# Performance work log

Measured on AMD Instinct MI355X. Metric: run time of the kernel, lower is better.

The kernel has to match this reference:

```python
import math
import jax, jax.numpy as jnp
import numpy as np

B = 32
L_ENC = 1024
LABEL = 512
PRED = 512
L_DEC = LABEL + PRED
ENC_IN = 7
C_OUT = 7
MARK = 4
D_MODEL = 512
N_HEADS = 8
D_FF = 2048
N_ENC = 2
N_DEC = 1
FACTOR = 1
MA = 25


def setup_inputs() -> dict:
    key = jax.random.key(0)
    ks = iter(jax.random.split(key, 40))
    def g(shape, scale=0.02):
        return jax.random.normal(next(ks), shape, dtype=jnp.float32) * scale
    inp = {}
    inp["x_enc"] = jax.random.normal(next(ks), (B, L_ENC, ENC_IN), dtype=jnp.float32)
    inp["x_mark_enc"] = jax.random.normal(next(ks), (B, L_ENC, MARK), dtype=jnp.float32)
    inp["x_dec"] = jax.random.normal(next(ks), (B, L_DEC, ENC_IN), dtype=jnp.float32)
    inp["x_mark_dec"] = jax.random.normal(next(ks), (B, L_DEC, MARK), dtype=jnp.float32)
    inp["W_enc_tok"] = g((3, ENC_IN, D_MODEL))
    inp["W_enc_tem"] = g((MARK, D_MODEL))
    inp["W_dec_tok"] = g((3, ENC_IN, D_MODEL))
    inp["W_dec_tem"] = g((MARK, D_MODEL))
    inp["enc_attn_W"] = g((N_ENC, 4, D_MODEL, D_MODEL))
    inp["enc_attn_b"] = jnp.zeros((N_ENC, 4, D_MODEL), jnp.float32)
    inp["enc_ff1"] = g((N_ENC, D_MODEL, D_FF))
    inp["enc_ff2"] = g((N_ENC, D_FF, D_MODEL))
    inp["enc_ln_w"] = jnp.ones((D_MODEL,), jnp.float32)
    inp["enc_ln_b"] = jnp.zeros((D_MODEL,), jnp.float32)
    inp["dec_self_W"] = g((N_DEC, 4, D_MODEL, D_MODEL))
    inp["dec_self_b"] = jnp.zeros((N_DEC, 4, D_MODEL), jnp.float32)
    inp["dec_cross_W"] = g((N_DEC, 4, D_MODEL, D_MODEL))
    inp["dec_cross_b"] = jnp.zeros((N_DEC, 4, D_MODEL), jnp.float32)
    inp["dec_ff1"] = g((N_DEC, D_MODEL, D_FF))
    inp["dec_ff2"] = g((N_DEC, D_FF, D_MODEL))
    inp["dec_trend_W"] = g((N_DEC, 3, D_MODEL, C_OUT))
    inp["dec_ln_w"] = jnp.ones((D_MODEL,), jnp.float32)
    inp["dec_ln_b"] = jnp.zeros((D_MODEL,), jnp.float32)
    inp["proj_W"] = g((D_MODEL, C_OUT))
    inp["proj_b"] = jnp.zeros((C_OUT,), jnp.float32)
    return inp


def moving_mean(x, k):
    # AvgPool1d(kernel=k, stride=1) over time with edge-replication padding (k odd)
    pad = (k - 1) // 2
    xp = jnp.concatenate([jnp.repeat(x[:, :1], pad, axis=1), x, jnp.repeat(x[:, -1:], pad, axis=1)], axis=1)
    cs = jnp.concatenate([jnp.zeros_like(xp[:, :1]), jnp.cumsum(xp, axis=1)], axis=1)
    return (cs[:, k:] - cs[:, :-k]) / k


def series_decomp(x, k=MA):
    m = moving_mean(x, k)
    return x - m, m


def my_layernorm(x, w, b):
    # LayerNorm over features, then subtract per-series seasonal bias (mean over time)
    mu = jnp.mean(x, axis=-1, keepdims=True)
    var = jnp.var(x, axis=-1, keepdims=True)
    xh = (x - mu) / jnp.sqrt(var + 1e-5) * w + b
    return xh - jnp.mean(xh, axis=1, keepdims=True)


def circ_conv3(x, W):
    # Conv1d kernel=3, circular padding, no bias; W: (3, c_in, c_out)
    xp = jnp.concatenate([x[:, -1:], x, x[:, :1]], axis=1)
    return xp[:, :-2] @ W[0] + xp[:, 1:-1] @ W[1] + xp[:, 2:] @ W[2]


def autocorrelation(q, k, v):
    # q: (B,L,H,E); k,v: (B,S,H,E)
    B_, L, H, E = q.shape
    S = v.shape[1]
    if L > S:
        pad = jnp.zeros((B_, L - S, H, E), q.dtype)
        k = jnp.concatenate([k, pad], axis=1)
        v = jnp.concatenate([v, pad], axis=1)
    else:
        k = k[:, :L]
        v = v[:, :L]
    qf = jnp.fft.rfft(jnp.transpose(q, (0, 2, 3, 1)), axis=-1)
    kf = jnp.fft.rfft(jnp.transpose(k, (0, 2, 3, 1)), axis=-1)
    corr = jnp.fft.irfft(qf * jnp.conj(kf), n=L, axis=-1)  # (B,H,E,L)
    vals = jnp.transpose(v, (0, 2, 3, 1))  # (B,H,E,L)
    top_k = int(FACTOR * math.log(L))
    mean_value = jnp.mean(corr, axis=(1, 2))  # (B,L)
    weights, delay = jax.lax.top_k(mean_value, top_k)
    tmp_corr = jax.nn.softmax(weights, axis=-1)  # (B,top_k)
    t_idx = jnp.arange(L)
    out = jnp.zeros_like(vals)
    for i in range(top_k):  # small fixed loop (top_k ~ log L)
        idx = (t_idx[None, :] + delay[:, i:i + 1]) % L  # (B,L) circular roll indices
        pat = jnp.take_along_axis(vals, idx[:, None, None, :], axis=-1)
        out = out + pat * tmp_corr[:, i][:, None, None, None]
    return jnp.transpose(out, (0, 3, 1, 2))  # (B,L,H,E)


def attn_layer(xq, xk, xv, W, b):
    Bq, L, _ = xq.shape
    S = xk.shape[1]
    q = (xq @ W[0] + b[0]).reshape(Bq, L, N_HEADS, -1)
    k = (xk @ W[1] + b[1]).reshape(Bq, S, N_HEADS, -1)
    v = (xv @ W[2] + b[2]).reshape(Bq, S, N_HEADS, -1)
    o = autocorrelation(q, k, v).reshape(Bq, L, -1)
    return o @ W[3] + b[3]


def reference(x_enc, x_mark_enc, x_dec, x_mark_dec, W_enc_tok, W_enc_tem, W_dec_tok, W_dec_tem, enc_attn_W, enc_attn_b, enc_ff1, enc_ff2, enc_ln_w, enc_ln_b, dec_self_W, dec_self_b, dec_cross_W, dec_cross_b, dec_ff1, dec_ff2, dec_trend_W, dec_ln_w, dec_ln_b, proj_W, proj_b):
    mean = jnp.broadcast_to(jnp.mean(x_enc, axis=1, keepdims=True), (x_enc.shape[0], PRED, x_enc.shape[2]))
    zeros = jnp.zeros((x_dec.shape[0], PRED, x_dec.shape[2]), x_enc.dtype)
    seasonal_init, trend_init = series_decomp(x_enc)
    trend_init = jnp.concatenate([trend_init[:, -LABEL:], mean], axis=1)
    seasonal_init = jnp.concatenate([seasonal_init[:, -LABEL:], zeros], axis=1)
    # embeddings (token conv + timeF linear; dropout=0 -> identity)
    enc = circ_conv3(x_enc, W_enc_tok) + x_mark_enc @ W_enc_tem
    for l in range(N_ENC):
        enc = enc + attn_layer(enc, enc, enc, enc_attn_W[l], enc_attn_b[l])
        enc, _ = series_decomp(enc)
        y = jax.nn.gelu(enc @ enc_ff1[l], approximate=False) @ enc_ff2[l]
        enc, _ = series_decomp(enc + y)
    enc = my_layernorm(enc, enc_ln_w, enc_ln_b)
    dec = circ_conv3(seasonal_init, W_dec_tok) + x_mark_dec @ W_dec_tem
    trend = trend_init
    for l in range(N_DEC):
        dec = dec + attn_layer(dec, dec, dec, dec_self_W[l], dec_self_b[l])
        dec, t1 = series_decomp(dec)
        dec = dec + attn_layer(dec, enc, enc, dec_cross_W[l], dec_cross_b[l])
        dec, t2 = series_decomp(dec)
        y = jax.nn.gelu(dec @ dec_ff1[l], approximate=False) @ dec_ff2[l]
        dec, t3 = series_decomp(dec + y)
        trend = trend + circ_conv3(t1 + t2 + t3, dec_trend_W[l])
    dec = my_layernorm(dec, dec_ln_w, dec_ln_b)
    seasonal = dec @ proj_W + proj_b
    return (trend + seasonal)[:, -PRED:]
```

## Files before the change

kernel.cpp:

```cpp
#include <hip/hip_runtime.h>

typedef unsigned short ushortb;
typedef __attribute__((ext_vector_type(8))) _Float16 f16x8;
typedef __attribute__((ext_vector_type(4))) float f32x4;

__device__ __forceinline__ float h2f(ushortb u) {
    _Float16 h; __builtin_memcpy(&h, &u, 2); return (float)h;
}
__device__ __forceinline__ ushortb f2h(float f) {
    _Float16 h = (_Float16)f; ushortb u; __builtin_memcpy(&u, &h, 2); return u;
}
__device__ __forceinline__ float gelu_f(float x) {
    float z = x * (1.59576912f + 0.0713548128f * x * x);
    return x / (1.f + __expf(-z));
}

__device__ __forceinline__ void ld16(const void* g, void* l) {
    __builtin_amdgcn_global_load_lds(
        (const __attribute__((address_space(1))) unsigned int*)g,
        (__attribute__((address_space(3))) unsigned int*)l, 16, 0, 0);
}

__device__ __forceinline__ void xcd_remap(int& bx, int& by) {
    int nx = gridDim.x;
    int total = nx * gridDim.y;
    bx = blockIdx.x; by = blockIdx.y;
    if ((total & 7) == 0) {
        int lin = by * nx + bx;
        int lin2 = (lin & 7) * (total >> 3) + (lin >> 3);
        by = lin2 / nx; bx = lin2 % nx;
    }
}

__launch_bounds__(256)
__global__ void gemm_h3(const ushortb* __restrict__ Ah, const ushortb* __restrict__ Al,
                        int lda,
                        const ushortb* __restrict__ Bh, const ushortb* __restrict__ Bl,
                        int ldb,
                        const float* __restrict__ bias,
                        ushortb* __restrict__ Ch, ushortb* __restrict__ Cl, int K)
{
    __shared__ __align__(16) ushortb LDS[16384];
    int bxs, bys; xcd_remap(bxs, bys);
    const int tid = threadIdx.x;
    const int wv = tid >> 6, ln = tid & 63;
    const int fr = ln & 15, fq = ln >> 4;
    const int m0 = bys << 7, n0 = bxs << 7;
    const int wr = (wv & 1) << 6, wc = (wv >> 1) << 6;

    const ushortb* gb; int ld;
    if (wv == 0)      { gb = Ah; ld = lda; }
    else if (wv == 1) { gb = Al; ld = lda; }
    else if (wv == 2) { gb = Bh; ld = ldb; }
    else              { gb = Bl; ld = ldb; }
    const int rbase = (wv < 2) ? m0 : n0;
    const ushortb* gp = gb + (size_t)(rbase + (ln >> 2)) * ld + (ln & 3) * 8;
    ushortb* lplane = LDS + wv * 4096;
    const size_t rstep = (size_t)ld << 4;

    f32x4 acc[4][4] = {};
    for (int k0 = 0; k0 < K; k0 += 32) {
        __syncthreads();
        #pragma unroll
        for (int i = 0; i < 8; ++i)
            ld16(gp + (size_t)i * rstep, lplane + i * 512);
        gp += 32;
        __syncthreads();
        f16x8 afh[4], afl[4], bfh[4], bfl[4];
        #pragma unroll
        for (int t = 0; t < 4; ++t) {
            int ra = ((wr + t*16 + fr) << 5) + (fq << 3);
            int rb = ((wc + t*16 + fr) << 5) + (fq << 3);
            afh[t] = *(const f16x8*)(const void*)(LDS + ra);
            afl[t] = *(const f16x8*)(const void*)(LDS + 4096 + ra);
            bfh[t] = *(const f16x8*)(const void*)(LDS + 8192 + rb);
            bfl[t] = *(const f16x8*)(const void*)(LDS + 12288 + rb);
        }
        #pragma unroll
        for (int tm = 0; tm < 4; ++tm)
            #pragma unroll
            for (int tn = 0; tn < 4; ++tn) {
                f32x4 c = acc[tm][tn];
                c = __builtin_amdgcn_mfma_f32_16x16x32_f16(afh[tm], bfh[tn], c, 0, 0, 0);
                c = __builtin_amdgcn_mfma_f32_16x16x32_f16(afl[tm], bfh[tn], c, 0, 0, 0);
                c = __builtin_amdgcn_mfma_f32_16x16x32_f16(afh[tm], bfl[tn], c, 0, 0, 0);
                acc[tm][tn] = c;
            }
    }
    const size_t bb = (size_t)(m0 >> 10) * 1048576;
    #pragma unroll
    for (int tm = 0; tm < 4; ++tm)
        #pragma unroll
        for (int tn = 0; tn < 4; ++tn) {
            int row0 = m0 + wr + tm*16 + fq*4;
            int col  = n0 + wc + tn*16 + fr;
            float bset = bias ? bias[col] : 0.f;
            int trow0 = row0 & 1023;
            size_t off = bb + (size_t)col * 1024 + trow0;
            float v0 = acc[tm][tn][0] + bset;
            float v1 = acc[tm][tn][1] + bset;
            float v2 = acc[tm][tn][2] + bset;
            float v3 = acc[tm][tn][3] + bset;
            ushortb h0 = f2h(v0), h1 = f2h(v1), h2v = f2h(v2), h3v = f2h(v3);
            uint2 hp, lp_;
            hp.x  = (unsigned)h0 | ((unsigned)h1 << 16);
            hp.y  = (unsigned)h2v | ((unsigned)h3v << 16);
            lp_.x = (unsigned)f2h(v0 - h2f(h0))  | ((unsigned)f2h(v1 - h2f(h1))  << 16);
            lp_.y = (unsigned)f2h(v2 - h2f(h2v)) | ((unsigned)f2h(v3 - h2f(h3v)) << 16);
            *(uint2*)(void*)(Ch + off) = hp;
            *(uint2*)(void*)(Cl + off) = lp_;
        }
}

__launch_bounds__(256)
__global__ void gemm_h1(const ushortb* __restrict__ Ah, int lda,
                        const ushortb* __restrict__ Bh, int ldb,
                        const float* __restrict__ bias,
                        const ushortb* __restrict__ Rh, const ushortb* __restrict__ Rl,
                        ushortb* __restrict__ Ch, ushortb* __restrict__ Cl,
                        int ldc, int K, int act)
{
    __shared__ __align__(16) ushortb LDS[8192];
    int bxs, bys; xcd_remap(bxs, bys);
    const int tid = threadIdx.x;
    const int wv = tid >> 6, ln = tid & 63;
    const int fr = ln & 15, fq = ln >> 4;
    const int m0 = bys << 7, n0 = bxs << 7;
    const int wr = (wv & 1) << 6, wc = (wv >> 1) << 6;

    const ushortb* gb; int ld; int rb;
    if (wv < 2) { gb = Ah; ld = lda; rb = m0; }
    else        { gb = Bh; ld = ldb; rb = n0; }
    const int half = wv & 1;
    const ushortb* gp = gb + (size_t)(rb + half*64 + (ln >> 2)) * ld + (ln & 3) * 8;
    ushortb* lp = LDS + (wv >> 1) * 4096 + half * 2048;
    const size_t rstep = (size_t)ld << 4;

    f32x4 acc[4][4] = {};
    for (int k0 = 0; k0 < K; k0 += 32) {
        __syncthreads();
        #pragma unroll
        for (int i = 0; i < 4; ++i)
            ld16(gp + (size_t)i * rstep, lp + i * 512);
        gp += 32;
        __syncthreads();
        f16x8 af[4], bf[4];
        #pragma unroll
        for (int t = 0; t < 4; ++t) {
            int ra = ((wr + t*16 + fr) << 5) + (fq << 3);
            int rx = ((wc + t*16 + fr) << 5) + (fq << 3);
            af[t] = *(const f16x8*)(const void*)(LDS + ra);
            bf[t] = *(const f16x8*)(const void*)(LDS + 4096 + rx);
        }
        #pragma unroll
        for (int tm = 0; tm < 4; ++tm)
            #pragma unroll
            for (int tn = 0; tn < 4; ++tn)
                acc[tm][tn] = __builtin_amdgcn_mfma_f32_16x16x32_f16(bf[tn], af[tm], acc[tm][tn], 0, 0, 0);
    }
    #pragma unroll
    for (int tm = 0; tm < 4; ++tm)
        #pragma unroll
        for (int tn = 0; tn < 4; ++tn) {
            int row  = m0 + wr + tm*16 + fr;
            int col0 = n0 + wc + tn*16 + (fq << 2);
            size_t off = (size_t)row * ldc + col0;
            float v0 = acc[tm][tn][0], v1 = acc[tm][tn][1];
            float v2 = acc[tm][tn][2], v3 = acc[tm][tn][3];
            if (bias) {
                float4 bv = *(const float4*)(bias + col0);
                v0 += bv.x; v1 += bv.y; v2 += bv.z; v3 += bv.w;
            }
            if (Rh) {
                uint2 rh = *(const uint2*)(const void*)(Rh + off);
                uint2 rl = *(const uint2*)(const void*)(Rl + off);
                v0 += h2f((ushortb)(rh.x & 0xFFFFu)) + h2f((ushortb)(rl.x & 0xFFFFu));
                v1 += h2f((ushortb)(rh.x >> 16))     + h2f((ushortb)(rl.x >> 16));
                v2 += h2f((ushortb)(rh.y & 0xFFFFu)) + h2f((ushortb)(rl.y & 0xFFFFu));
                v3 += h2f((ushortb)(rh.y >> 16))     + h2f((ushortb)(rl.y >> 16));
            }
            if (act) { v0 = gelu_f(v0); v1 = gelu_f(v1); v2 = gelu_f(v2); v3 = gelu_f(v3); }
            ushortb h0 = f2h(v0), h1 = f2h(v1), h2v = f2h(v2), h3v = f2h(v3);
            uint2 hp;
            hp.x = (unsigned)h0 | ((unsigned)h1 << 16);
            hp.y = (unsigned)h2v | ((unsigned)h3v << 16);
            *(uint2*)(void*)(Ch + off) = hp;
            if (Cl) {
                uint2 lo;
                lo.x = (unsigned)f2h(v0 - h2f(h0))  | ((unsigned)f2h(v1 - h2f(h1))  << 16);
                lo.y = (unsigned)f2h(v2 - h2f(h2v)) | ((unsigned)f2h(v3 - h2f(h3v)) << 16);
                *(uint2*)(void*)(Cl + off) = lo;
            }
        }
}

__launch_bounds__(256)
__global__ void gemm_og(const ushortb* __restrict__ Vh,
                        const int* __restrict__ DELAY, const float* __restrict__ WGT,
                        const ushortb* __restrict__ Bh, int ldb,
                        const float* __restrict__ bias,
                        const ushortb* __restrict__ Rh, const ushortb* __restrict__ Rl,
                        ushortb* __restrict__ Ch, ushortb* __restrict__ Cl,
                        int ldc, int K)
{
    __shared__ __align__(16) ushortb LDS[8192];
    int bxs, bys; xcd_remap(bxs, bys);
    const int tid = threadIdx.x;
    const int wv = tid >> 6, ln = tid & 63;
    const int fr = ln & 15, fq = ln >> 4;
    const int m0 = bys << 7, n0 = bxs << 7;
    const int wr = (wv & 1) << 6, wc = (wv >> 1) << 6;
    const int half = wv & 1;

    const int b = m0 >> 10;
    const ushortb* Vb = Vh + ((size_t)b << 19);
    int del[6]; float w6[6];
    #pragma unroll
    for (int j = 0; j < 6; ++j) { del[j] = DELAY[b*6+j]; w6[j] = WGT[b*6+j]; }

    const ushortb* gp = Bh + (size_t)(n0 + half*64 + (ln >> 2)) * ldb + (ln & 3) * 8;
    ushortb* lp = LDS + (wv >> 1) * 4096 + half * 2048;
    const size_t rstep = (size_t)ldb << 4;

    f32x4 acc[4][4] = {};
    for (int k0 = 0; k0 < K; k0 += 32) {
        __syncthreads();
        if (wv < 2) {
            #pragma unroll
            for (int i = 0; i < 4; ++i) {
                int t = (m0 + half*64 + (ln >> 2) + 16*i) & 1023;
                float a0=0,a1=0,a2=0,a3=0,a4=0,a5=0,a6=0,a7=0;
                #pragma unroll
                for (int j = 0; j < 6; ++j) {
                    int s = (t + del[j]) & 1023;
                    f16x8 hv = *(const f16x8*)(const void*)(Vb + (((size_t)s) << 9) + k0 + ((ln & 3) << 3));
                    float w = w6[j];
                    a0 += w * (float)hv[0]; a1 += w * (float)hv[1];
                    a2 += w * (float)hv[2]; a3 += w * (float)hv[3];
                    a4 += w * (float)hv[4]; a5 += w * (float)hv[5];
                    a6 += w * (float)hv[6]; a7 += w * (float)hv[7];
                }
                f16x8 ov;
                ov[0]=(_Float16)a0; ov[1]=(_Float16)a1; ov[2]=(_Float16)a2; ov[3]=(_Float16)a3;
                ov[4]=(_Float16)a4; ov[5]=(_Float16)a5; ov[6]=(_Float16)a6; ov[7]=(_Float16)a7;
                *(f16x8*)(void*)(lp + i*512 + ln*8) = ov;
            }
        } else {
            #pragma unroll
            for (int i = 0; i < 4; ++i)
                ld16(gp + (size_t)i * rstep, lp + i * 512);
            gp += 32;
        }
        __syncthreads();
        f16x8 af[4], bf[4];
        #pragma unroll
        for (int t = 0; t < 4; ++t) {
            int ra = ((wr + t*16 + fr) << 5) + (fq << 3);
            int rx = ((wc + t*16 + fr) << 5) + (fq << 3);
            af[t] = *(const f16x8*)(const void*)(LDS + ra);
            bf[t] = *(const f16x8*)(const void*)(LDS + 4096 + rx);
        }
        #pragma unroll
        for (int tm = 0; tm < 4; ++tm)
            #pragma unroll
            for (int tn = 0; tn < 4; ++tn)
                acc[tm][tn] = __builtin_amdgcn_mfma_f32_16x16x32_f16(bf[tn], af[tm], acc[tm][tn], 0, 0, 0);
    }
    #pragma unroll
    for (int tm = 0; tm < 4; ++tm)
        #pragma unroll
        for (int tn = 0; tn < 4; ++tn) {
            int row  = m0 + wr + tm*16 + fr;
            int col0 = n0 + wc + tn*16 + (fq << 2);
            size_t off = (size_t)row * ldc + col0;
            float4 bv = *(const float4*)(bias + col0);
            float v0 = acc[tm][tn][0] + bv.x, v1 = acc[tm][tn][1] + bv.y;
            float v2 = acc[tm][tn][2] + bv.z, v3 = acc[tm][tn][3] + bv.w;
            uint2 rh = *(const uint2*)(const void*)(Rh + off);
            uint2 rl = *(const uint2*)(const void*)(Rl + off);
            v0 += h2f((ushortb)(rh.x & 0xFFFFu)) + h2f((ushortb)(rl.x & 0xFFFFu));
            v1 += h2f((ushortb)(rh.x >> 16))     + h2f((ushortb)(rl.x >> 16));
            v2 += h2f((ushortb)(rh.y & 0xFFFFu)) + h2f((ushortb)(rl.y & 0xFFFFu));
            v3 += h2f((ushortb)(rh.y >> 16))     + h2f((ushortb)(rl.y >> 16));
            ushortb h0 = f2h(v0), h1 = f2h(v1), h2v = f2h(v2), h3v = f2h(v3);
            uint2 hp, lo;
            hp.x = (unsigned)h0 | ((unsigned)h1 << 16);
            hp.y = (unsigned)h2v | ((unsigned)h3v << 16);
            lo.x = (unsigned)f2h(v0 - h2f(h0))  | ((unsigned)f2h(v1 - h2f(h1))  << 16);
            lo.y = (unsigned)f2h(v2 - h2f(h2v)) | ((unsigned)f2h(v3 - h2f(h3v)) << 16);
            *(uint2*)(void*)(Ch + off) = hp;
            *(uint2*)(void*)(Cl + off) = lo;
        }
}

__device__ __forceinline__ void fft1024_tw(float* Xr, float* Xi, float* Yr, float* Yi,
                                           int tid, const float* csf, const float* snf)
{
    float *psr = Xr, *psi = Xi, *pdr = Yr, *pdi = Yi;
    #pragma unroll
    for (int st = 0; st < 10; ++st) {
        const int s = 1 << st;
        #pragma unroll
        for (int h = 0; h < 2; ++h) {
            int u = tid + (h << 8);
            int qq = u & (s - 1);
            int ps = u - qq;
            float cs = csf[st*2+h], sn = snf[st*2+h];
            float ar = psr[u],       ai = psi[u];
            float br = psr[u + 512], bi = psi[u + 512];
            int d1 = qq + (ps << 1);
            pdr[d1] = ar + br;  pdi[d1] = ai + bi;
            float tr = ar - br, ti = ai - bi;
            pdr[d1 + s] = tr * cs - ti * sn;
            pdi[d1 + s] = tr * sn + ti * cs;
        }
        __syncthreads();
        float* t0 = psr; psr = pdr; pdr = t0;
        float* t1 = psi; psi = pdi; pdi = t1;
    }
}

__launch_bounds__(256)
__global__ void corr_fft(const ushortb* __restrict__ QKh, const ushortb* __restrict__ QKl,
                         float* __restrict__ SP)
{
    __shared__ float Xr[1024], Xi[1024], Yr[1024], Yi[1024];
    const int tid = threadIdx.x;
    const int c = blockIdx.x, b = blockIdx.y;
    const size_t bbase = (size_t)b << 20;
    float csf[20], snf[20];
    #pragma unroll
    for (int st = 0; st < 10; ++st) {
        const int s = 1 << st;
        #pragma unroll
        for (int h = 0; h < 2; ++h) {
            int u = tid + (h << 8);
            int ps = u - (u & (s - 1));
            float ang = -(3.14159265358979323846f / 512.f) * (float)ps;
            __sincosf(ang, &snf[st*2+h], &csf[st*2+h]);
        }
    }
    float sr[4] = {0.f, 0.f, 0.f, 0.f};
    float si[4] = {0.f, 0.f, 0.f, 0.f};
    for (int j = 0; j < 16; ++j) {
        int d = (c << 4) + j;
        const ushortb* qh = QKh + bbase + ((size_t)d << 10);
        const ushortb* ql = QKl + bbase + ((size_t)d << 10);
        const ushortb* kh = qh + (512u << 10);
        const ushortb* kl = ql + (512u << 10);
        __syncthreads();
        #pragma unroll
        for (int i = 0; i < 4; ++i) {
            int t = tid + (i << 8);
            Xr[t] = h2f(qh[t]) + h2f(ql[t]);
            Xi[t] = h2f(kh[t]) + h2f(kl[t]);
        }
        __syncthreads();
        fft1024_tw(Xr, Xi, Yr, Yi, tid, csf, snf);
        #pragma unroll
        for (int i = 0; i < 4; ++i) {
            int f  = tid + (i << 8);
            int f2 = (1024 - f) & 1023;
            float axr = Xr[f],  axi = Xi[f];
            float cxr = Xr[f2], cxi = -Xi[f2];
            float ur = axr + cxr, ui = axi + cxi;
            float vr = axr - cxr, vi = -(axi - cxi);
            float wr_ = ur * vr - ui * vi;
            float wi_ = ur * vi + ui * vr;
            sr[i] += -0.25f * wi_;
            si[i] +=  0.25f * wr_;
        }
    }
    const size_t base = ((size_t)(b * 32 + c)) << 11;
    #pragma unroll
    for (int i = 0; i < 4; ++i) {
        int f = tid + (i << 8);
        SP[base + f]        = sr[i];
        SP[base + 1024 + f] = si[i];
    }
}

__launch_bounds__(256)
__global__ void topk6f_fft(const float* __restrict__ SP, int* __restrict__ DELAY,
                           float* __restrict__ WGT)
{
    __shared__ float Xr[1024], Xi[1024], Yr[1024], Yi[1024];
    __shared__ float v[1024];
    __shared__ float rv[256];
    __shared__ int   ri[256];
    __shared__ float wv6[6];
    __shared__ int   wi6[6];
    const int b = blockIdx.x, tid = threadIdx.x;
    float csf[20], snf[20];
    #pragma unroll
    for (int st = 0; st < 10; ++st) {
        const int s = 1 << st;
        #pragma unroll
        for (int h = 0; h < 2; ++h) {
            int u = tid + (h << 8);
            int ps = u - (u & (s - 1));
            float ang = (3.14159265358979323846f / 512.f) * (float)ps;
            __sincosf(ang, &snf[st*2+h], &csf[st*2+h]);
        }
    }
    #pragma unroll
    for (int i = 0; i < 4; ++i) {
        int f = tid + (i << 8);
        float ar = 0.f, ai = 0.f;
        for (int c = 0; c < 32; ++c) {
            size_t base = ((size_t)(b * 32 + c)) << 11;
            ar += SP[base + f];
            ai += SP[base + 1024 + f];
        }
        Xr[f] = ar; Xi[f] = ai;
    }
    __syncthreads();
    fft1024_tw(Xr, Xi, Yr, Yi, tid, csf, snf);
    #pragma unroll
    for (int i = 0; i < 4; ++i) {
        int f = tid + (i << 8);
        v[f] = Xr[f] * (1.f / 524288.f);
    }
    __syncthreads();
    for (int it = 0; it < 6; ++it) {
        float best = v[tid]; int bi = tid;
        #pragma unroll
        for (int k = 1; k < 4; ++k) {
            int i = tid + (k << 8);
            float xv = v[i];
            if (xv > best) { best = xv; bi = i; }
        }
        rv[tid] = best; ri[tid] = bi;
        __syncthreads();
        for (int s = 128; s > 0; s >>= 1) {
            if (tid < s) {
                if (rv[tid+s] > rv[tid] || (rv[tid+s] == rv[tid] && ri[tid+s] < ri[tid])) {
                    rv[tid] = rv[tid+s]; ri[tid] = ri[tid+s];
                }
            }
            __syncthreads();
        }
        if (tid == 0) { wv6[it] = rv[0]; wi6[it] = ri[0]; v[ri[0]] = -1e30f; }
        __syncthreads();
    }
    if (tid == 0) {
        float mx = wv6[0], s = 0.f, e[6];
        #pragma unroll
        for (int i = 0; i < 6; ++i) { e[i] = expf(wv6[i] - mx); s += e[i]; }
        #pragma unroll
        for (int i = 0; i < 6; ++i) { WGT[b*6+i] = e[i]/s; DELAY[b*6+i] = wi6[i]; }
    }
}

__launch_bounds__(256)
__global__ void decomp512v(const ushortb* __restrict__ Xh, const ushortb* __restrict__ Xl,
                           ushortb* __restrict__ Sh, ushortb* __restrict__ Sl,
                           float* __restrict__ TTs, int tmode)
{
    int idx = blockIdx.x * 256 + threadIdx.x;
    int d0 = (idx & 127) << 2, bt = idx >> 7, t = bt & 1023;
    int base = bt - t;
    float s0=0,s1=0,s2=0,s3=0;
    #pragma unroll
    for (int w = -12; w <= 12; ++w) {
        int tt = t + w; tt = tt < 0 ? 0 : (tt > 1023 ? 1023 : tt);
        size_t ro = ((size_t)(base + tt) << 9) + d0;
        uint2 hv = *(const uint2*)(Xh + ro);
        uint2 lv = *(const uint2*)(Xl + ro);
        s0 += h2f((ushortb)(hv.x & 0xFFFFu)) + h2f((ushortb)(lv.x & 0xFFFFu));
        s1 += h2f((ushortb)(hv.x >> 16))     + h2f((ushortb)(lv.x >> 16));
        s2 += h2f((ushortb)(hv.y & 0xFFFFu)) + h2f((ushortb)(lv.y & 0xFFFFu));
        s3 += h2f((ushortb)(hv.y >> 16))     + h2f((ushortb)(lv.y >> 16));
    }
    float m0 = s0*(1.f/25.f), m1 = s1*(1.f/25.f), m2 = s2*(1.f/25.f), m3 = s3*(1.f/25.f);
    size_t co = ((size_t)bt << 9) + d0;
    uint2 chv = *(const uint2*)(Xh + co);
    uint2 clv = *(const uint2*)(Xl + co);
    float v0 = h2f((ushortb)(chv.x & 0xFFFFu)) + h2f((ushortb)(clv.x & 0xFFFFu)) - m0;
    float v1 = h2f((ushortb)(chv.x >> 16))     + h2f((ushortb)(clv.x >> 16))     - m1;
    float v2 = h2f((ushortb)(chv.y & 0xFFFFu)) + h2f((ushortb)(clv.y & 0xFFFFu)) - m2;
    float v3 = h2f((ushortb)(chv.y >> 16))     + h2f((ushortb)(clv.y >> 16))     - m3;
    ushortb h0=f2h(v0), h1=f2h(v1), h2v=f2h(v2), h3=f2h(v3);
    uint2 hp, lp;
    hp.x = (unsigned)h0 | ((unsigned)h1 << 16); hp.y = (unsigned)h2v | ((unsigned)h3 << 16);
    lp.x = (unsigned)f2h(v0-h2f(h0)) | ((unsigned)f2h(v1-h2f(h1)) << 16);
    lp.y = (unsigned)f2h(v2-h2f(h2v)) | ((unsigned)f2h(v3-h2f(h3)) << 16);
    *(uint2*)(Sh + co) = hp; *(uint2*)(Sl + co) = lp;
    if (tmode) {
        int slot = (t >= 511) ? (t - 511) : (t == 0 ? 513 : -1);
        if (slot >= 0) {
            int b = bt >> 10;
            float* tp = TTs + (size_t)b * 263168 + ((size_t)slot << 9) + d0;
            if (tmode == 1) { tp[0]=m0; tp[1]=m1; tp[2]=m2; tp[3]=m3; }
            else            { tp[0]+=m0; tp[1]+=m1; tp[2]+=m2; tp[3]+=m3; }
        }
    }
}

__launch_bounds__(256)
__global__ void ln_rows(const ushortb* __restrict__ Xh, const ushortb* __restrict__ Xl,
                        const float* __restrict__ w, const float* __restrict__ bias,
                        ushortb* __restrict__ Yh, ushortb* __restrict__ Yl)
{
    __shared__ float r1[256], r2[256];
    const int row = blockIdx.x, tid = threadIdx.x;
    size_t ro = (size_t)row * 512;
    float x0 = h2f(Xh[ro + tid]) + h2f(Xl[ro + tid]);
    float x1 = h2f(Xh[ro + tid + 256]) + h2f(Xl[ro + tid + 256]);
    r1[tid] = x0 + x1; r2[tid] = x0*x0 + x1*x1;
    __syncthreads();
    for (int s = 128; s > 0; s >>= 1) {
        if (tid < s) { r1[tid] += r1[tid+s]; r2[tid] += r2[tid+s]; }
        __syncthreads();
    }
    float mu = r1[0] * (1.f/512.f);
    float var = r2[0] * (1.f/512.f) - mu*mu;
    float rstd = rsqrtf(var + 1e-5f);
    float v0 = (x0 - mu) * rstd * w[tid]     + bias[tid];
    float v1 = (x1 - mu) * rstd * w[tid+256] + bias[tid+256];
    ushortb h0 = f2h(v0), h1 = f2h(v1);
    Yh[ro + tid] = h0;       Yl[ro + tid] = f2h(v0 - h2f(h0));
    Yh[ro + tid + 256] = h1; Yl[ro + tid + 256] = f2h(v1 - h2f(h1));
}

__launch_bounds__(256)
__global__ void colmean_p(const ushortb* __restrict__ Yh, const ushortb* __restrict__ Yl,
                          float* __restrict__ PC)
{
    int i = blockIdx.x * 256 + threadIdx.x;
    int b = i >> 12, r = i & 4095, d = r >> 3, c = r & 7;
    size_t o = ((size_t)b << 19) + ((size_t)(c << 7) << 9) + d;
    float s = 0.f;
    for (int t = 0; t < 128; ++t) { size_t oo = o + ((size_t)t << 9); s += h2f(Yh[oo]) + h2f(Yl[oo]); }
    PC[i] = s * (1.f/1024.f);
}

__launch_bounds__(256)
__global__ void submean_s(const ushortb* __restrict__ Yh, const ushortb* __restrict__ Yl,
                          const float* __restrict__ PC,
                          ushortb* __restrict__ Zh, ushortb* __restrict__ Zl)
{
    int idx = blockIdx.x * 256 + threadIdx.x;
    int d = idx & 511, b = idx >> 19;
    const float* pc = PC + ((size_t)b << 12) + (d << 3);
    float m = ((pc[0]+pc[1])+(pc[2]+pc[3]))+((pc[4]+pc[5])+(pc[6]+pc[7]));
    float v = h2f(Yh[idx]) + h2f(Yl[idx]) - m;
    ushortb h = f2h(v);
    Zh[idx] = h; Zl[idx] = f2h(v - h2f(h));
}

__launch_bounds__(256)
__global__ void embed_es(const float* __restrict__ x, const float* __restrict__ mark,
                         const float* __restrict__ Wtok, const float* __restrict__ Wtem,
                         ushortb* __restrict__ Oh, ushortb* __restrict__ Ol)
{
    int idx = blockIdx.x * 256 + threadIdx.x;
    int d = idx & 511, bt = idx >> 9, t = bt & 1023, b = bt >> 10;
    float acc = 0.f;
    #pragma unroll
    for (int j = 0; j < 3; ++j) {
        int tt = (t + 1023 + j) & 1023;
        const float* xr = x + (size_t)(b*1024 + tt)*7;
        #pragma unroll
        for (int c = 0; c < 7; ++c)
            acc += xr[c] * Wtok[(j*7+c)*512 + d];
    }
    const float* mr = mark + (size_t)bt*4;
    #pragma unroll
    for (int m = 0; m < 4; ++m) acc += mr[m] * Wtem[m*512 + d];
    ushortb h = f2h(acc);
    Oh[idx] = h; Ol[idx] = f2h(acc - h2f(h));
}

__launch_bounds__(256)
__global__ void mean7(const float* __restrict__ x, float* __restrict__ M7)
{
    __shared__ float r[256];
    int bc = blockIdx.x, b = bc / 7, c = bc % 7, tid = threadIdx.x;
    float s = 0.f;
    for (int t = tid; t < 1024; t += 256) s += x[(size_t)(b*1024+t)*7 + c];
    r[tid] = s; __syncthreads();
    for (int st = 128; st > 0; st >>= 1) { if (tid < st) r[tid] += r[tid+st]; __syncthreads(); }
    if (tid == 0) M7[bc] = r[0] * (1.f/1024.f);
}

__launch_bounds__(256)
__global__ void decomp7(const float* __restrict__ x, const float* __restrict__ M7,
                        float* __restrict__ SEAS7, float* __restrict__ TREND7)
{
    int idx = blockIdx.x * 256 + threadIdx.x;
    int c = idx % 7, bt = idx / 7, t = bt & 1023, b = bt >> 10;
    if (t < 512) {
        int s0 = t + 512;
        float s = 0.f;
        #pragma unroll
        for (int w = -12; w <= 12; ++w) {
            int tt = s0 + w; tt = tt < 0 ? 0 : (tt > 1023 ? 1023 : tt);
            s += x[(size_t)(b*1024+tt)*7 + c];
        }
        float m = s * (1.f/25.f);
        SEAS7[idx] = x[(size_t)(b*1024+s0)*7 + c] - m;
        TREND7[idx] = m;
    } else {
        SEAS7[idx] = 0.f;
        TREND7[idx] = M7[b*7 + c];
    }
}

__launch_bounds__(256)
__global__ void final_fused(const ushortb* __restrict__ Xh, const ushortb* __restrict__ Xl,
                            const float* __restrict__ PW, const float* __restrict__ PB,
                            const float* __restrict__ TW, const float* __restrict__ TTs,
                            const float* __restrict__ TREND7, float* __restrict__ out)
{
    __shared__ float WT[10752];
    __shared__ float WP[3584];
    for (int i = threadIdx.x; i < 10752; i += 256) WT[i] = TW[i];
    for (int i = threadIdx.x; i < 3584; i += 256) WP[i] = PW[i];
    __syncthreads();
    int idx = blockIdx.x * 256 + threadIdx.x;
    int c = idx % 7, btt = idx / 7, tt = btt & 511, b = btt >> 9;
    int t = tt + 512;
    float acc = PB[c] + TREND7[(size_t)(b*1024 + t)*7 + c];
    size_t ro = ((size_t)(b*1024 + t) << 9);
    for (int d = 0; d < 512; ++d)
        acc += (h2f(Xh[ro + d]) + h2f(Xl[ro + d])) * WP[d*7 + c];
    for (int j = 0; j < 3; ++j) {
        int t2 = t - 1 + j;
        int slot = (t2 >= 1024) ? 513 : (t2 - 511);
        const float* r = TTs + (size_t)b * 263168 + ((size_t)slot << 9);
        const float* wj = WT + j*3584 + c;
        for (int d = 0; d < 512; ++d) acc += r[d] * wj[d*7];
    }
    out[idx] = acc;
}

__launch_bounds__(256)
__global__ void wsplit_att(const float* __restrict__ W, ushortb* __restrict__ pool, int which)
{
    __shared__ float t[32][33];
    const int m = blockIdx.z;
    const int kb = blockIdx.y << 5, nb = blockIdx.x << 5;
    const int c = threadIdx.x & 31, rr = threadIdx.x >> 5;
    const float* Wm = W + (size_t)m * 262144;
    #pragma unroll
    for (int i = 0; i < 4; ++i)
        t[rr + i*8][c] = Wm[(size_t)(kb + rr + i*8) * 512 + nb + c];
    __syncthreads();
    const int a = (which == 0) ? (m >> 2) : (which + 1);
    const int j = (which == 0) ? (m & 3) : m;
    size_t hi, lo; bool haslo;
    if (j == 0)      { hi = 0;       lo = 524288; haslo = true; }
    else if (j == 1) { hi = 262144;  lo = 786432; haslo = true; }
    else if (j == 2) { hi = 1048576; lo = 0; haslo = false; }
    else             { hi = 1310720; lo = 0; haslo = false; }
    ushortb* pb = pool + (size_t)a * 1572864;
    #pragma unroll
    for (int i = 0; i < 4; ++i) {
        int n = nb + rr + i*8, k = kb + c;
        float v = t[c][rr + i*8];
        ushortb h = f2h(v);
        pb[hi + (size_t)n * 512 + k] = h;
        if (haslo) pb[lo + (size_t)n * 512 + k] = f2h(v - h2f(h));
    }
}

__launch_bounds__(256)
__global__ void wsplit_ff(const float* __restrict__ W, ushortb* __restrict__ dh,
                          int K, int N)
{
    __shared__ float t[32][33];
    const int m = blockIdx.z;
    const int kb = blockIdx.y << 5, nb = blockIdx.x << 5;
    const int c = threadIdx.x & 31, rr = threadIdx.x >> 5;
    const float* Wm = W + (size_t)m * K * N;
    #pragma unroll
    for (int i = 0; i < 4; ++i)
        t[rr + i*8][c] = Wm[(size_t)(kb + rr + i*8) * N + nb + c];
    __syncthreads();
    ushortb* Dh = dh + (size_t)m * 1048576;
    #pragma unroll
    for (int i = 0; i < 4; ++i) {
        int n = nb + rr + i*8, k = kb + c;
        Dh[(size_t)n * K + k] = f2h(t[c][rr + i*8]);
    }
}

__launch_bounds__(256)
__global__ void sentinel(float* __restrict__ out, int n)
{
    int i = blockIdx.x * 256 + threadIdx.x;
    if (i < n) out[i] = -54321.0f;
}

extern "C" void kernel_launch(void* const* d_in, const int* in_sizes, int n_in,
                              void* d_out, int out_size, void* d_ws, size_t ws_size,
                              hipStream_t stream)
{
    const float* x_enc      = (const float*)d_in[0];
    const float* x_mark_enc = (const float*)d_in[1];
    const float* x_mark_dec = (const float*)d_in[3];
    const float* W_enc_tok  = (const float*)d_in[4];
    const float* W_enc_tem  = (const float*)d_in[5];
    const float* W_dec_tok  = (const float*)d_in[6];
    const float* W_dec_tem  = (const float*)d_in[7];
    const float* enc_attn_W = (const float*)d_in[8];
    const float* enc_attn_b = (const float*)d_in[9];
    const float* enc_ff1    = (const float*)d_in[10];
    const float* enc_ff2    = (const float*)d_in[11];
    const float* enc_ln_w   = (const float*)d_in[12];
    const float* enc_ln_b   = (const float*)d_in[13];
    const float* dec_self_W = (const float*)d_in[14];
    const float* dec_self_b = (const float*)d_in[15];
    const float* dec_cross_W= (const float*)d_in[16];
    const float* dec_cross_b= (const float*)d_in[17];
    const float* dec_ff1    = (const float*)d_in[18];
    const float* dec_ff2    = (const float*)d_in[19];
    const float* dec_trend_W= (const float*)d_in[20];
    const float* dec_ln_w   = (const float*)d_in[21];
    const float* dec_ln_b   = (const float*)d_in[22];
    const float* proj_W     = (const float*)d_in[23];
    const float* proj_b     = (const float*)d_in[24];
    float* out = (float*)d_out;

    const size_t ATT_E = (size_t)4 * 1572864;
    const size_t FF_E  = (size_t)3 * 1048576;
    const size_t WBYTES = (ATT_E + 2 * FF_E) * 2 + 4096;

    auto need = [&](long g) -> size_t {
        size_t TGl = (size_t)g * 1024;
        size_t pairs = 3 * TGl * 2048;
        size_t qk    = TGl * 4096;
        size_t vh    = TGl * 1024;
        size_t tts   = (size_t)g * 263168 * 4;
        size_t pbin  = (size_t)g * 262144;
        size_t misc  = (size_t)g * (16384 + 28 + 28672 + 28672 + 64) + 65536;
        return WBYTES + pairs + qk + vh + tts + pbin + misc + 16384;
    };
    int G = 0;
    for (int g = 32; g >= 1; g >>= 1) if (need(g) <= ws_size) { G = g; break; }
    if (G == 0) {
        sentinel<<<(out_size + 255) / 256, 256, 0, stream>>>(out, out_size);
        return;
    }
    const int TG = G * 1024;

    char* p = (char*)d_ws;
    auto carve = [&](size_t bytes) -> char* {
        char* r = p; p += (bytes + 255) & ~(size_t)255; return r;
    };
    ushortb* ATT = (ushortb*)carve(ATT_E * 2);
    ushortb* FF1 = (ushortb*)carve(FF_E * 2);
    ushortb* FF2 = (ushortb*)carve(FF_E * 2);

    const size_t SPLB = (size_t)TG * 512 * 2;
    ushortb* SAh = (ushortb*)carve(SPLB);
    ushortb* SAl = (ushortb*)carve(SPLB);
    ushortb* TMh = (ushortb*)carve(SPLB);
    ushortb* TMl = (ushortb*)carve(SPLB);
    ushortb* SEh = (ushortb*)carve(SPLB);
    ushortb* SEl = (ushortb*)carve(SPLB);
    char* R1 = carve((size_t)TG * 4096);
    ushortb* Vh = (ushortb*)carve((size_t)TG * 1024);
    float* TTs   = (float*)carve((size_t)G * 263168 * 4);
    float* PBIN  = (float*)carve((size_t)G * 262144);
    float* PC    = (float*)carve((size_t)G * 16384);
    float* M7    = (float*)carve((size_t)G * 28);
    float* SEAS7 = (float*)carve((size_t)G * 28672);
    float* TREND7= (float*)carve((size_t)G * 28672);
    float* WGT   = (float*)carve((size_t)G * 24);
    int*   DELAY = (int*)  carve((size_t)G * 24);

    ushortb* QKh = (ushortb*)R1;
    ushortb* QKl = QKh + (size_t)TG * 1024;
    ushortb* MIDh = (ushortb*)R1;

    wsplit_att<<<dim3(16,16,8),256,0,stream>>>(enc_attn_W, ATT, 0);
    wsplit_att<<<dim3(16,16,4),256,0,stream>>>(dec_self_W, ATT, 1);
    wsplit_att<<<dim3(16,16,4),256,0,stream>>>(dec_cross_W, ATT, 2);
    wsplit_ff<<<dim3(64,16,2),256,0,stream>>>(enc_ff1, FF1, 512, 2048);
    wsplit_ff<<<dim3(64,16,1),256,0,stream>>>(dec_ff1, FF1 + (size_t)2*1048576, 512, 2048);
    wsplit_ff<<<dim3(16,64,2),256,0,stream>>>(enc_ff2, FF2, 2048, 512);
    wsplit_ff<<<dim3(16,64,1),256,0,stream>>>(dec_ff2, FF2 + (size_t)2*1048576, 2048, 512);

    for (int g0 = 0; g0 < 32; g0 += G) {
        const float* xe  = x_enc      + (size_t)g0 * 1024 * 7;
        const float* me  = x_mark_enc + (size_t)g0 * 1024 * 4;
        const float* md  = x_mark_dec + (size_t)g0 * 1024 * 4;
        float*       outg= out        + (size_t)g0 * 512 * 7;
        const int GB = G * 8;

        auto corr_gather_oproj = [&](const ushortb* base, const float* bv,
                                     const ushortb* rh, const ushortb* rl) {
            corr_fft<<<dim3(32,G),256,0,stream>>>(QKh, QKl, PBIN);
            topk6f_fft<<<G,256,0,stream>>>(PBIN, DELAY, WGT);
            gemm_og<<<dim3(4,GB),256,0,stream>>>(Vh, DELAY, WGT,
                                                 base+1310720,512, bv+1536,
                                                 rh,rl, TMh,TMl, 512, 512);
        };
        auto attn_self = [&](const ushortb* xh, const ushortb* xl, int a, const float* bv) {
            const ushortb* base = ATT + (size_t)a * 1572864;
            gemm_h3<<<dim3(8,GB),256,0,stream>>>(xh,xl,512, base,base+524288,512, bv,
                                                 QKh,QKl, 512);
            gemm_h1<<<dim3(4,GB),256,0,stream>>>(xh,512, base+1048576,512, bv+1024,
                                                 nullptr,nullptr, Vh,nullptr, 512, 512, 0);
            corr_gather_oproj(base, bv, xh, xl);
        };
        auto attn_cross = [&](const ushortb* qh, const ushortb* ql,
                              const ushortb* kvh, const ushortb* kvl,
                              int a, const float* bv) {
            const ushortb* base = ATT + (size_t)a * 1572864;
            gemm_h3<<<dim3(4,GB),256,0,stream>>>(qh,ql,512, base,base+524288,512, bv,
                                                 QKh,QKl, 512);
            gemm_h3<<<dim3(4,GB),256,0,stream>>>(kvh,kvl,512, base+262144,base+786432,512, bv+512,
                                                 QKh+524288,QKl+524288, 512);
            gemm_h1<<<dim3(4,GB),256,0,stream>>>(kvh,512, base+1048576,512, bv+1024,
                                                 nullptr,nullptr, Vh,nullptr, 512, 512, 0);
            corr_gather_oproj(base, bv, qh, ql);
        };
        auto ffn = [&](const ushortb* xh, const ushortb* xl, int fi) {
            gemm_h1<<<dim3(16,GB),256,0,stream>>>(xh,512, FF1 + (size_t)fi*1048576,512, nullptr,
                                                  nullptr,nullptr, MIDh,nullptr, 2048, 512, 1);
            gemm_h1<<<dim3(4,GB),256,0,stream>>>(MIDh,2048, FF2 + (size_t)fi*1048576,2048, nullptr,
                                                 xh,xl, TMh,TMl, 512, 2048, 0);
        };

        embed_es<<<TG*2,256,0,stream>>>(xe, me, W_enc_tok, W_enc_tem, SAh, SAl);
        for (int l = 0; l < 2; ++l) {
            attn_self(SAh, SAl, l, enc_attn_b + (size_t)l*4*512);
            decomp512v<<<TG/2,256,0,stream>>>(TMh, TMl, SAh, SAl, nullptr, 0);
            ffn(SAh, SAl, l);
            decomp512v<<<TG/2,256,0,stream>>>(TMh, TMl, SAh, SAl, nullptr, 0);
        }
        ln_rows<<<TG,256,0,stream>>>(SAh, SAl, enc_ln_w, enc_ln_b, TMh, TMl);
        colmean_p<<<G*16,256,0,stream>>>(TMh, TMl, PC);
        submean_s<<<TG*2,256,0,stream>>>(TMh, TMl, PC, SEh, SEl);

        mean7<<<G*7,256,0,stream>>>(xe, M7);
        decomp7<<<G*28,256,0,stream>>>(xe, M7, SEAS7, TREND7);
        embed_es<<<TG*2,256,0,stream>>>(SEAS7, md, W_dec_tok, W_dec_tem, SAh, SAl);

        attn_self(SAh, SAl, 2, dec_self_b);
        decomp512v<<<TG/2,256,0,stream>>>(TMh, TMl, SAh, SAl, TTs, 1);

        attn_cross(SAh, SAl, SEh, SEl, 3, dec_cross_b);
        decomp512v<<<TG/2,256,0,stream>>>(TMh, TMl, SAh, SAl, TTs, 2);

        ffn(SAh, SAl, 2);
        decomp512v<<<TG/2,256,0,stream>>>(TMh, TMl, SAh, SAl, TTs, 2);

        ln_rows<<<TG,256,0,stream>>>(SAh, SAl, dec_ln_w, dec_ln_b, TMh, TMl);
        colmean_p<<<G*16,256,0,stream>>>(TMh, TMl, PC);
        submean_s<<<TG*2,256,0,stream>>>(TMh, TMl, PC, SAh, SAl);

        final_fused<<<G*14,256,0,stream>>>(SAh, SAl, proj_W, proj_b, dec_trend_W,
                                           TTs, TREND7, outg);
    }
}
```

Measured before the change: 3.923 ms.

## Swizzle GEMM LDS tiles and tile Q/K output layout for coalesced FFT loads

Applies an XOR swizzle to the k-chunk position of each row in the LDS staging tiles of all three GEMM kernels, on both the global-to-LDS copy and the fragment reads. The goal is to avoid bank conflicts on the 16-byte fragment reads. The gemm_h3 epilogue now writes Q/K in a tiled layout of 16-channel by 16-time blocks instead of channel-major rows, and corr_fft reads that layout with 8-byte vector loads and float4 LDS stores. This replaces scattered 2-byte loads, but ties the FFT kernel's input indexing to the new tile layout.

Result: slower. 4.615 ms (+17.7%).

```diff
diff --git a/kernel.cpp b/kernel.cpp
--- a/kernel.cpp
+++ b/kernel.cpp
@@ -32,6 +32,7 @@
     }
 }
 
+
 __launch_bounds__(256)
 __global__ void gemm_h3(const ushortb* __restrict__ Ah, const ushortb* __restrict__ Al,
                         int lda,
@@ -54,9 +55,11 @@
     else if (wv == 2) { gb = Bh; ld = ldb; }
     else              { gb = Bl; ld = ldb; }
     const int rbase = (wv < 2) ? m0 : n0;
-    const ushortb* gp = gb + (size_t)(rbase + (ln >> 2)) * ld + (ln & 3) * 8;
+    const ushortb* gp = gb + (size_t)(rbase + (ln >> 2)) * ld
+                          + (((ln & 3) ^ ((ln >> 3) & 3)) * 8);
     ushortb* lplane = LDS + wv * 4096;
     const size_t rstep = (size_t)ld << 4;
+    const int sw = (fr >> 1) & 3;
 
     f32x4 acc[4][4] = {};
     for (int k0 = 0; k0 < K; k0 += 32) {
@@ -69,8 +72,8 @@
         f16x8 afh[4], afl[4], bfh[4], bfl[4];
         #pragma unroll
         for (int t = 0; t < 4; ++t) {
-            int ra = ((wr + t*16 + fr) << 5) + (fq << 3);
-            int rb = ((wc + t*16 + fr) << 5) + (fq << 3);
+            int ra = ((wr + t*16 + fr) << 5) + ((fq ^ sw) << 3);
+            int rb = ((wc + t*16 + fr) << 5) + ((fq ^ sw) << 3);
             afh[t] = *(const f16x8*)(const void*)(LDS + ra);
             afl[t] = *(const f16x8*)(const void*)(LDS + 4096 + ra);
             bfh[t] = *(const f16x8*)(const void*)(LDS + 8192 + rb);
@@ -92,11 +95,11 @@
     for (int tm = 0; tm < 4; ++tm)
         #pragma unroll
         for (int tn = 0; tn < 4; ++tn) {
-            int row0 = m0 + wr + tm*16 + fq*4;
-            int col  = n0 + wc + tn*16 + fr;
+            int tqb = ((m0 + wr + tm*16) & 1023) >> 4;
+            int dg  = (n0 + wc + tn*16) >> 4;
+            int col = n0 + wc + tn*16 + fr;
             float bset = bias ? bias[col] : 0.f;
-            int trow0 = row0 & 1023;
-            size_t off = bb + (size_t)col * 1024 + trow0;
+            size_t off = bb + (size_t)dg * 16384 + tqb * 256 + ln * 4;
             float v0 = acc[tm][tn][0] + bset;
             float v1 = acc[tm][tn][1] + bset;
             float v2 = acc[tm][tn][2] + bset;
@@ -132,9 +135,11 @@
     if (wv < 2) { gb = Ah; ld = lda; rb = m0; }
     else        { gb = Bh; ld = ldb; rb = n0; }
     const int half = wv & 1;
-    const ushortb* gp = gb + (size_t)(rb + half*64 + (ln >> 2)) * ld + (ln & 3) * 8;
+    const ushortb* gp = gb + (size_t)(rb + half*64 + (ln >> 2)) * ld
+                          + (((ln & 3) ^ ((ln >> 3) & 3)) * 8);
     ushortb* lp = LDS + (wv >> 1) * 4096 + half * 2048;
     const size_t rstep = (size_t)ld << 4;
+    const int sw = (fr >> 1) & 3;
 
     f32x4 acc[4][4] = {};
     for (int k0 = 0; k0 < K; k0 += 32) {
@@ -147,8 +152,8 @@
         f16x8 af[4], bf[4];
         #pragma unroll
         for (int t = 0; t < 4; ++t) {
-            int ra = ((wr + t*16 + fr) << 5) + (fq << 3);
-            int rx = ((wc + t*16 + fr) << 5) + (fq << 3);
+            int ra = ((wr + t*16 + fr) << 5) + ((fq ^ sw) << 3);
+            int rx = ((wc + t*16 + fr) << 5) + ((fq ^ sw) << 3);
             af[t] = *(const f16x8*)(const void*)(LDS + ra);
             bf[t] = *(const f16x8*)(const void*)(LDS + 4096 + rx);
         }
@@ -218,9 +223,12 @@
     #pragma unroll
     for (int j = 0; j < 6; ++j) { del[j] = DELAY[b*6+j]; w6[j] = WGT[b*6+j]; }
 
-    const ushortb* gp = Bh + (size_t)(n0 + half*64 + (ln >> 2)) * ldb + (ln & 3) * 8;
+    const ushortb* gp = Bh + (size_t)(n0 + half*64 + (ln >> 2)) * ldb
+                           + (((ln & 3) ^ ((ln >> 3) & 3)) * 8);
     ushortb* lp = LDS + (wv >> 1) * 4096 + half * 2048;
     const size_t rstep = (size_t)ldb << 4;
+    const int sw = (fr >> 1) & 3;
+    const int adst = ((ln >> 2) << 5) + (((ln & 3) ^ ((ln >> 3) & 3)) << 3);
 
     f32x4 acc[4][4] = {};
     for (int k0 = 0; k0 < K; k0 += 32) {
@@ -243,7 +251,7 @@
                 f16x8 ov;
                 ov[0]=(_Float16)a0; ov[1]=(_Float16)a1; ov[2]=(_Float16)a2; ov[3]=(_Float16)a3;
                 ov[4]=(_Float16)a4; ov[5]=(_Float16)a5; ov[6]=(_Float16)a6; ov[7]=(_Float16)a7;
-                *(f16x8*)(void*)(lp + i*512 + ln*8) = ov;
+                *(f16x8*)(void*)(lp + i*512 + adst) = ov;
             }
         } else {
             #pragma unroll
@@ -255,8 +263,8 @@
         f16x8 af[4], bf[4];
         #pragma unroll
         for (int t = 0; t < 4; ++t) {
-            int ra = ((wr + t*16 + fr) << 5) + (fq << 3);
-            int rx = ((wc + t*16 + fr) << 5) + (fq << 3);
+            int ra = ((wr + t*16 + fr) << 5) + ((fq ^ sw) << 3);
+            int rx = ((wc + t*16 + fr) << 5) + ((fq ^ sw) << 3);
             af[t] = *(const f16x8*)(const void*)(LDS + ra);
             bf[t] = *(const f16x8*)(const void*)(LDS + 4096 + rx);
         }
@@ -324,7 +332,7 @@
 __global__ void corr_fft(const ushortb* __restrict__ QKh, const ushortb* __restrict__ QKl,
                          float* __restrict__ SP)
 {
-    __shared__ float Xr[1024], Xi[1024], Yr[1024], Yi[1024];
+    __shared__ __align__(16) float Xr[1024], Xi[1024], Yr[1024], Yi[1024];
     const int tid = threadIdx.x;
     const int c = blockIdx.x, b = blockIdx.y;
     const size_t bbase = (size_t)b << 20;
@@ -340,21 +348,32 @@
             __sincosf(ang, &snf[st*2+h], &csf[st*2+h]);
         }
     }
+    const int toff = ((tid >> 2) << 8) + ((tid & 3) << 6);
+    const int t0 = tid << 2;
     float sr[4] = {0.f, 0.f, 0.f, 0.f};
     float si[4] = {0.f, 0.f, 0.f, 0.f};
     for (int j = 0; j < 16; ++j) {
-        int d = (c << 4) + j;
-        const ushortb* qh = QKh + bbase + ((size_t)d << 10);
-        const ushortb* ql = QKl + bbase + ((size_t)d << 10);
-        const ushortb* kh = qh + (512u << 10);
-        const ushortb* kl = ql + (512u << 10);
-        __syncthreads();
-        #pragma unroll
-        for (int i = 0; i < 4; ++i) {
-            int t = tid + (i << 8);
-            Xr[t] = h2f(qh[t]) + h2f(ql[t]);
-            Xi[t] = h2f(kh[t]) + h2f(kl[t]);
-        }
+        size_t qoff = bbase + ((size_t)c << 14) + toff + (j << 2);
+        const ushortb* qh = QKh + qoff;
+        const ushortb* ql = QKl + qoff;
+        const ushortb* kh = qh + 524288;
+        const ushortb* kl = ql + 524288;
+        __syncthreads();
+        uint2 qa = *(const uint2*)(const void*)qh;
+        uint2 qb = *(const uint2*)(const void*)ql;
+        uint2 ka = *(const uint2*)(const void*)kh;
+        uint2 kb = *(const uint2*)(const void*)kl;
+        float4 xr, xi;
+        xr.x = h2f((ushortb)(qa.x & 0xFFFFu)) + h2f((ushortb)(qb.x & 0xFFFFu));
+        xr.y = h2f((ushortb)(qa.x >> 16))     + h2f((ushortb)(qb.x >> 16));
+        xr.z = h2f((ushortb)(qa.y & 0xFFFFu)) + h2f((ushortb)(qb.y & 0xFFFFu));
+        xr.w = h2f((ushortb)(qa.y >> 16))     + h2f((ushortb)(qb.y >> 16));
+        xi.x = h2f((ushortb)(ka.x & 0xFFFFu)) + h2f((ushortb)(kb.x & 0xFFFFu));
+        xi.y = h2f((ushortb)(ka.x >> 16))     + h2f((ushortb)(kb.x >> 16));
+        xi.z = h2f((ushortb)(ka.y & 0xFFFFu)) + h2f((ushortb)(kb.y & 0xFFFFu));
+        xi.w = h2f((ushortb)(ka.y >> 16))     + h2f((ushortb)(kb.y >> 16));
+        *(float4*)(Xr + t0) = xr;
+        *(float4*)(Xi + t0) = xi;
         __syncthreads();
         fft1024_tw(Xr, Xi, Yr, Yi, tid, csf, snf);
         #pragma unroll
```

## XOR-swizzle GEMM LDS tiles and stage transposed h3 epilogue through LDS

Applied to the files above, without the earlier changes.

Applies an XOR swizzle to the 16-byte chunk index used by the global-to-LDS loads and the fragment reads in three GEMM kernels, so the 64-byte LDS rows no longer cause bank conflicts on the f16x8 fragment loads. In gemm_h3 the transposed output store, which wrote scattered 8-byte pieces with a 1024-element column stride, is replaced by staging each column block in padded LDS and then writing contiguous row segments per column. This aims to cut LDS bank conflicts and uncoalesced global writes, at the cost of extra barriers and LDS traffic in the epilogue.

Result: no change. 3.933 ms (+0.3%).

```diff
diff --git a/kernel.cpp b/kernel.cpp
--- a/kernel.cpp
+++ b/kernel.cpp
@@ -32,6 +32,7 @@
     }
 }
 
+
 __launch_bounds__(256)
 __global__ void gemm_h3(const ushortb* __restrict__ Ah, const ushortb* __restrict__ Al,
                         int lda,
@@ -54,9 +55,11 @@
     else if (wv == 2) { gb = Bh; ld = ldb; }
     else              { gb = Bl; ld = ldb; }
     const int rbase = (wv < 2) ? m0 : n0;
-    const ushortb* gp = gb + (size_t)(rbase + (ln >> 2)) * ld + (ln & 3) * 8;
+    const ushortb* gp = gb + (size_t)(rbase + (ln >> 2)) * ld
+                          + (((ln & 3) ^ ((ln >> 3) & 3)) * 8);
     ushortb* lplane = LDS + wv * 4096;
     const size_t rstep = (size_t)ld << 4;
+    const int sw = (fr >> 1) & 3;
 
     f32x4 acc[4][4] = {};
     for (int k0 = 0; k0 < K; k0 += 32) {
@@ -69,8 +72,8 @@
         f16x8 afh[4], afl[4], bfh[4], bfl[4];
         #pragma unroll
         for (int t = 0; t < 4; ++t) {
-            int ra = ((wr + t*16 + fr) << 5) + (fq << 3);
-            int rb = ((wc + t*16 + fr) << 5) + (fq << 3);
+            int ra = ((wr + t*16 + fr) << 5) + ((fq ^ sw) << 3);
+            int rb = ((wc + t*16 + fr) << 5) + ((fq ^ sw) << 3);
             afh[t] = *(const f16x8*)(const void*)(LDS + ra);
             afl[t] = *(const f16x8*)(const void*)(LDS + 4096 + ra);
             bfh[t] = *(const f16x8*)(const void*)(LDS + 8192 + rb);
@@ -88,15 +91,20 @@
             }
     }
     const size_t bb = (size_t)(m0 >> 10) * 1048576;
-    #pragma unroll
-    for (int tm = 0; tm < 4; ++tm)
-        #pragma unroll
-        for (int tn = 0; tn < 4; ++tn) {
-            int row0 = m0 + wr + tm*16 + fq*4;
-            int col  = n0 + wc + tn*16 + fr;
-            float bset = bias ? bias[col] : 0.f;
-            int trow0 = row0 & 1023;
-            size_t off = bb + (size_t)col * 1024 + trow0;
+    const int trow0 = m0 & 1023;
+    const int PS = 4224;
+    ushortb* EH = LDS;
+    ushortb* EL = LDS + PS;
+    const int cl  = ((wv >> 1) << 4) + fr;
+    const int rcl = tid >> 3, seg = tid & 7;
+    #pragma unroll
+    for (int tn = 0; tn < 4; ++tn) {
+        __syncthreads();
+        int col = n0 + ((wv >> 1) << 6) + tn*16 + fr;
+        float bset = bias ? bias[col] : 0.f;
+        #pragma unroll
+        for (int tm = 0; tm < 4; ++tm) {
+            int tl = ((wv & 1) << 6) + tm*16 + (fq << 2);
             float v0 = acc[tm][tn][0] + bset;
             float v1 = acc[tm][tn][1] + bset;
             float v2 = acc[tm][tn][2] + bset;
@@ -107,9 +115,20 @@
             hp.y  = (unsigned)h2v | ((unsigned)h3v << 16);
             lp_.x = (unsigned)f2h(v0 - h2f(h0))  | ((unsigned)f2h(v1 - h2f(h1))  << 16);
             lp_.y = (unsigned)f2h(v2 - h2f(h2v)) | ((unsigned)f2h(v3 - h2f(h3v)) << 16);
-            *(uint2*)(void*)(Ch + off) = hp;
-            *(uint2*)(void*)(Cl + off) = lp_;
-        }
+            *(uint2*)(void*)(EH + cl*132 + tl) = hp;
+            *(uint2*)(void*)(EL + cl*132 + tl) = lp_;
+        }
+        __syncthreads();
+        int gcol = n0 + ((rcl >> 4) << 6) + tn*16 + (rcl & 15);
+        size_t goff = bb + (size_t)gcol * 1024 + trow0 + (seg << 4);
+        const ushortb* sh = EH + rcl*132 + (seg << 4);
+        const ushortb* sl = EL + rcl*132 + (seg << 4);
+        #pragma unroll
+        for (int i = 0; i < 4; ++i) {
+            *(uint2*)(void*)(Ch + goff + i*4) = *(const uint2*)(const void*)(sh + i*4);
+            *(uint2*)(void*)(Cl + goff + i*4) = *(const uint2*)(const void*)(sl + i*4);
+        }
+    }
 }
 
 __launch_bounds__(256)
@@ -132,9 +151,11 @@
     if (wv < 2) { gb = Ah; ld = lda; rb = m0; }
     else        { gb = Bh; ld = ldb; rb = n0; }
     const int half = wv & 1;
-    const ushortb* gp = gb + (size_t)(rb + half*64 + (ln >> 2)) * ld + (ln & 3) * 8;
+    const ushortb* gp = gb + (size_t)(rb + half*64 + (ln >> 2)) * ld
+                          + (((ln & 3) ^ ((ln >> 3) & 3)) * 8);
     ushortb* lp = LDS + (wv >> 1) * 4096 + half * 2048;
     const size_t rstep = (size_t)ld << 4;
+    const int sw = (fr >> 1) & 3;
 
     f32x4 acc[4][4] = {};
     for (int k0 = 0; k0 < K; k0 += 32) {
@@ -147,8 +168,8 @@
         f16x8 af[4], bf[4];
         #pragma unroll
         for (int t = 0; t < 4; ++t) {
-            int ra = ((wr + t*16 + fr) << 5) + (fq << 3);
-            int rx = ((wc + t*16 + fr) << 5) + (fq << 3);
+            int ra = ((wr + t*16 + fr) << 5) + ((fq ^ sw) << 3);
+            int rx = ((wc + t*16 + fr) << 5) + ((fq ^ sw) << 3);
             af[t] = *(const f16x8*)(const void*)(LDS + ra);
             bf[t] = *(const f16x8*)(const void*)(LDS + 4096 + rx);
         }
@@ -218,9 +239,12 @@
     #pragma unroll
     for (int j = 0; j < 6; ++j) { del[j] = DELAY[b*6+j]; w6[j] = WGT[b*6+j]; }
 
-    const ushortb* gp = Bh + (size_t)(n0 + half*64 + (ln >> 2)) * ldb + (ln & 3) * 8;
+    const ushortb* gp = Bh + (size_t)(n0 + half*64 + (ln >> 2)) * ldb
+                           + (((ln & 3) ^ ((ln >> 3) & 3)) * 8);
     ushortb* lp = LDS + (wv >> 1) * 4096 + half * 2048;
     const size_t rstep = (size_t)ldb << 4;
+    const int sw = (fr >> 1) & 3;
+    const int adst = ((ln >> 2) << 5) + (((ln & 3) ^ ((ln >> 3) & 3)) << 3);
 
     f32x4 acc[4][4] = {};
     for (int k0 = 0; k0 < K; k0 += 32) {
@@ -243,7 +267,7 @@
                 f16x8 ov;
                 ov[0]=(_Float16)a0; ov[1]=(_Float16)a1; ov[2]=(_Float16)a2; ov[3]=(_Float16)a3;
                 ov[4]=(_Float16)a4; ov[5]=(_Float16)a5; ov[6]=(_Float16)a6; ov[7]=(_Float16)a7;
-                *(f16x8*)(void*)(lp + i*512 + ln*8) = ov;
+                *(f16x8*)(void*)(lp + i*512 + adst) = ov;
             }
         } else {
             #pragma unroll
@@ -255,8 +279,8 @@
         f16x8 af[4], bf[4];
         #pragma unroll
         for (int t = 0; t < 4; ++t) {
-            int ra = ((wr + t*16 + fr) << 5) + (fq << 3);
-            int rx = ((wc + t*16 + fr) << 5) + (fq << 3);
+            int ra = ((wr + t*16 + fr) << 5) + ((fq ^ sw) << 3);
+            int rx = ((wc + t*16 + fr) << 5) + ((fq ^ sw) << 3);
             af[t] = *(const f16x8*)(const void*)(LDS + ra);
             bf[t] = *(const f16x8*)(const void*)(LDS + 4096 + rx);
         }
```
